# Kernel optimization log

Measured on AMD Instinct MI355X. Metric: run time of the kernel, lower is better.

Reference implementation:

```python
import jax, jax.numpy as jnp
import numpy as np

N_EMBDS = 1024
N_HEADS = 16
HEAD_DIM = N_EMBDS // N_HEADS


def setup_inputs() -> dict:
    key = jax.random.key(0)
    ks = jax.random.split(key, 5)
    B, T, C = 2, 2048, N_EMBDS
    x = jax.random.normal(ks[0], (B, T, C), dtype=jnp.float32)
    s = 1.0 / np.sqrt(C)
    W_attn = jax.random.normal(ks[1], (C, 3 * C), dtype=jnp.float32) * s
    b_attn = jnp.zeros((3 * C,), dtype=jnp.float32)
    W_proj = jax.random.normal(ks[2], (C, C), dtype=jnp.float32) * s
    b_proj = jnp.zeros((C,), dtype=jnp.float32)
    return {"x": x, "W_attn": W_attn, "b_attn": b_attn, "W_proj": W_proj, "b_proj": b_proj}


def reference(x, W_attn, b_attn, W_proj, b_proj):
    B, T, C = x.shape
    H, D = N_HEADS, HEAD_DIM
    qkv = x @ W_attn + b_attn  # [B, T, 3C]
    q, k, v = jnp.split(qkv, 3, axis=-1)
    # [B, H, T, D]
    q = q.reshape(B, T, H, D).transpose(0, 2, 1, 3)
    k = k.reshape(B, T, H, D).transpose(0, 2, 1, 3)
    v = v.reshape(B, T, H, D).transpose(0, 2, 1, 3)
    att = jnp.einsum('bhqd,bhkd->bhqk', q, k) * (1.0 / np.sqrt(D))  # [B,H,T,T]
    causal = jnp.tril(jnp.ones((T, T), dtype=bool))
    att = jnp.where(causal[None, None], att, -jnp.inf)
    att = jax.nn.softmax(att, axis=-1)
    y = jnp.einsum('bhqk,bhkd->bhqd', att, v)  # [B,H,T,D]
    y = y.transpose(0, 2, 1, 3).reshape(B, T, C)
    return y @ W_proj + b_proj
```

## Files before the change

### kernel.cpp

```cpp
#include <hip/hip_runtime.h>
#include <hip/hip_bf16.h>


typedef __bf16 bf16x8 __attribute__((ext_vector_type(8)));
typedef float  f32x4  __attribute__((ext_vector_type(4)));
#define BF16 __hip_bfloat16

constexpr int Bb = 2, Tt = 2048, Cc = 1024, Hh = 16, Dd = 64;
constexpr float NEG_INF = -1e30f;

__device__ __forceinline__ f32x4 mfma16(bf16x8 a, bf16x8 b, f32x4 c) {
  return __builtin_amdgcn_mfma_f32_16x16x32_bf16(a, b, c, 0, 0, 0);
}

__device__ __forceinline__ void gll16(const void* g, void* l) {
  __builtin_amdgcn_global_load_lds((const __attribute__((address_space(1))) void*)g,
                                   (__attribute__((address_space(3))) void*)l,
                                   16, 0, 0);
}

__device__ __forceinline__ int swz64(int r, int c) {
  return r * 64 + ((((c >> 3) ^ r) & 7) << 3) + (c & 7);
}

__device__ __forceinline__ int kperm(int kr) {
  return (((kr >> 5) << 1) + ((kr >> 2) & 1)) * 16 + (((kr >> 3) & 3) << 2) + (kr & 3);
}

__global__ void prep_kernel(const float* __restrict__ x, BF16* __restrict__ xb,
                            const float* __restrict__ Wa, BF16* __restrict__ WaT,
                            const float* __restrict__ Wp, BF16* __restrict__ WpT) {
  __shared__ float tile[32][33];
  const int bx = blockIdx.x, tid = threadIdx.x;
  if (bx < 2048) {
    const int i = (bx * 256 + tid) * 8;
    const float4 a = *(const float4*)&x[i];
    const float4 b = *(const float4*)&x[i + 4];
    BF16 o[8];
    o[0] = __float2bfloat16(a.x); o[1] = __float2bfloat16(a.y);
    o[2] = __float2bfloat16(a.z); o[3] = __float2bfloat16(a.w);
    o[4] = __float2bfloat16(b.x); o[5] = __float2bfloat16(b.y);
    o[6] = __float2bfloat16(b.z); o[7] = __float2bfloat16(b.w);
    *(uint4*)&xb[i] = *(const uint4*)o;
    return;
  }
  const float* in; BF16* outT; int K, N, gx, gy;
  if (bx < 5120) {
    const int idx = bx - 2048;
    in = Wa; outT = WaT; K = 1024; N = 3072; gx = idx % 96; gy = idx / 96;
  } else {
    const int idx = bx - 5120;
    in = Wp; outT = WpT; K = 1024; N = 1024; gx = idx % 32; gy = idx / 32;
  }
  const int n0 = gx * 32, k0 = gy * 32;
  const int tx = tid & 31, ty = tid >> 5;
#pragma unroll
  for (int i = ty; i < 32; i += 8) tile[i][tx] = in[(size_t)(k0 + i) * N + (n0 + tx)];
  __syncthreads();
#pragma unroll
  for (int i = ty; i < 32; i += 8)
    outT[(size_t)(n0 + i) * K + (k0 + tx)] = __float2bfloat16(tile[tx][i]);
}

__global__ void transpose_v(const BF16* __restrict__ in, BF16* __restrict__ out) {
  __shared__ BF16 tile[32][33];
  const int t0 = blockIdx.x * 32, d0 = blockIdx.y * 32, bh = blockIdx.z;
  const BF16* src = in + (size_t)bh * Tt * Dd;
  BF16* dst = out + (size_t)bh * Tt * Dd;
  const int tx = threadIdx.x, ty = threadIdx.y;
#pragma unroll
  for (int i = ty; i < 32; i += 8) tile[i][tx] = src[(size_t)(t0 + i) * Dd + (d0 + tx)];
  __syncthreads();
#pragma unroll
  for (int i = ty; i < 32; i += 8) dst[(size_t)(d0 + i) * Tt + (t0 + tx)] = tile[tx][i];
}

template <int MODE>
__global__ __launch_bounds__(256) void gemm_bt(const BF16* __restrict__ A,
                                               const BF16* __restrict__ Bt,
                                               const float* __restrict__ bias,
                                               BF16* __restrict__ oq,
                                               BF16* __restrict__ ok,
                                               BF16* __restrict__ ov,
                                               float* __restrict__ fout,
                                               int Ndim, int Kdim) {
  __shared__ alignas(16) BF16 sA[128 * 32];
  __shared__ alignas(16) BF16 sB[128 * 32];
  const int tid = threadIdx.x;
  const int wave = tid >> 6, lane = tid & 63;
  const int quad = lane >> 4, l16 = lane & 15;
  const int wm = (wave >> 1) * 64, wn = (wave & 1) * 64;
  const int bm = blockIdx.y * 128, bn = blockIdx.x * 128;

  f32x4 acc[4][4];
#pragma unroll
  for (int i = 0; i < 4; ++i)
#pragma unroll
    for (int j = 0; j < 4; ++j) acc[i][j] = f32x4{0.f, 0.f, 0.f, 0.f};

  const int rowA = wave * 32 + (lane >> 2);
  const int sub8 = (lane & 3) * 8;
  const BF16* gA0 = &A[(size_t)(bm + rowA) * Kdim + sub8];
  const BF16* gB0 = &Bt[(size_t)(bn + rowA) * Kdim + sub8];
  const size_t rstep16 = (size_t)16 * Kdim;
  BF16* lA0 = &sA[wave * 1024];
  BF16* lA1 = &sA[wave * 1024 + 512];
  BF16* lB0 = &sB[wave * 1024];
  BF16* lB1 = &sB[wave * 1024 + 512];

  for (int k0 = 0; k0 < Kdim; k0 += 32) {
    __syncthreads();
    gll16(gA0 + k0, lA0);
    gll16(gA0 + rstep16 + k0, lA1);
    gll16(gB0 + k0, lB0);
    gll16(gB0 + rstep16 + k0, lB1);
    __syncthreads();

    bf16x8 af[4], bf_[4];
#pragma unroll
    for (int i = 0; i < 4; ++i)
      af[i] = *(const bf16x8*)&sA[(wm + i * 16 + l16) * 32 + quad * 8];
#pragma unroll
    for (int j = 0; j < 4; ++j)
      bf_[j] = *(const bf16x8*)&sB[(wn + j * 16 + l16) * 32 + quad * 8];
#pragma unroll
    for (int i = 0; i < 4; ++i)
#pragma unroll
      for (int j = 0; j < 4; ++j) acc[i][j] = mfma16(af[i], bf_[j], acc[i][j]);
  }

#pragma unroll
  for (int j = 0; j < 4; ++j) {
    const int gn = bn + wn + j * 16 + l16;
    const float bsv = bias[gn];
#pragma unroll
    for (int i = 0; i < 4; ++i) {
#pragma unroll
      for (int r = 0; r < 4; ++r) {
        const int gm = bm + wm + i * 16 + quad * 4 + r;
        float val = acc[i][j][r] + bsv;
        if (MODE == 0) {
          const int which = gn >> 10, c = gn & 1023;
          const int hh = c >> 6, dd = c & 63;
          const int bb = gm >> 11, tk = gm & 2047;
          if (which == 0) val *= 0.125f;
          BF16* dst = (which == 0) ? oq : (which == 1) ? ok : ov;
          dst[(((size_t)(bb * Hh + hh)) * Tt + tk) * Dd + dd] = __float2bfloat16(val);
        } else {
          fout[(size_t)gm * Ndim + gn] = val;
        }
      }
    }
  }
}

__global__ __launch_bounds__(256) void attn_kernel(const BF16* __restrict__ qg,
                                                   const BF16* __restrict__ kg,
                                                   const BF16* __restrict__ vtg,
                                                   BF16* __restrict__ yb) {
  __shared__ alignas(16) BF16 sK[64 * 64];
  __shared__ alignas(16) BF16 sV[64 * 64];
  const int pr = blockIdx.x, h = blockIdx.y, b = blockIdx.z;
  const int qt[2] = {pr, 31 - pr};
  const int tid = threadIdx.x;
  const int wave = tid >> 6, lane = tid & 63;
  const int quad = lane >> 4, l16 = lane & 15;
  const size_t base = ((size_t)(b * Hh + h)) * Tt * Dd;

  bf16x8 qf[2][2];
#pragma unroll
  for (int s = 0; s < 2; ++s) {
    const size_t off = base + (size_t)(qt[s] * 64 + wave * 16 + l16) * Dd;
    qf[s][0] = *(const bf16x8*)&qg[off + quad * 8];
    qf[s][1] = *(const bf16x8*)&qg[off + 32 + quad * 8];
  }

  bf16x8 ones8;
#pragma unroll
  for (int j = 0; j < 8; ++j) ones8[j] = (__bf16)1.0f;

  f32x4 o[2][4], oL[2];
#pragma unroll
  for (int s = 0; s < 2; ++s) {
#pragma unroll
    for (int i = 0; i < 4; ++i) o[s][i] = f32x4{0.f, 0.f, 0.f, 0.f};
    oL[s] = f32x4{0.f, 0.f, 0.f, 0.f};
  }

  const int krow = tid >> 2, kcg = (tid & 3) * 16;
  const int kprow = kperm(krow);

  for (int jt = 0; jt <= qt[1]; ++jt) {
    const int kb = jt * 64;
    __syncthreads();
    {
      const uint4* pk = (const uint4*)&kg[base + (size_t)(kb + krow) * Dd + kcg];
      const uint4* pv = (const uint4*)&vtg[base + (size_t)krow * Tt + kb + kcg];
      uint4 k0 = pk[0], k1 = pk[1];
      uint4 v0 = pv[0], v1 = pv[1];
      *(uint4*)&sK[swz64(kprow, kcg)]     = k0;
      *(uint4*)&sK[swz64(kprow, kcg + 8)] = k1;
      *(uint4*)&sV[swz64(krow, kcg)]      = v0;
      *(uint4*)&sV[swz64(krow, kcg + 8)]  = v1;
    }
    __syncthreads();

    const bool actA = (jt <= qt[0]);

    f32x4 sS[2][4];
#pragma unroll
    for (int t = 0; t < 4; ++t) {
      const bf16x8 kf0 = *(const bf16x8*)&sK[swz64(t * 16 + l16, quad * 8)];
      const bf16x8 kf1 = *(const bf16x8*)&sK[swz64(t * 16 + l16, 32 + quad * 8)];
      sS[1][t] = mfma16(kf0, qf[1][0], f32x4{0.f, 0.f, 0.f, 0.f});
      sS[1][t] = mfma16(kf1, qf[1][1], sS[1][t]);
      if (actA) {
        sS[0][t] = mfma16(kf0, qf[0][0], f32x4{0.f, 0.f, 0.f, 0.f});
        sS[0][t] = mfma16(kf1, qf[0][1], sS[0][t]);
      }
    }

    bf16x8 pf[2][2];
#pragma unroll
    for (int s = 0; s < 2; ++s) {
      if (s == 0 && !actA) continue;
      if (jt == qt[s]) {
        const int q = qt[s] * 64 + wave * 16 + l16;
#pragma unroll
        for (int t = 0; t < 4; ++t) {
          const int kc0 = kb + (t >> 1) * 32 + quad * 8 + (t & 1) * 4;
#pragma unroll
          for (int r = 0; r < 4; ++r)
            if (kc0 + r > q) sS[s][t][r] = NEG_INF;
        }
      }
#pragma unroll
      for (int cc = 0; cc < 2; ++cc)
#pragma unroll
        for (int j = 0; j < 8; ++j)
          pf[s][cc][j] = (__bf16)__expf(sS[s][cc * 2 + (j >> 2)][j & 3] - 12.0f);
    }

#pragma unroll
    for (int cc = 0; cc < 2; ++cc) {
#pragma unroll
      for (int dt = 0; dt < 4; ++dt) {
        const bf16x8 vb =
            *(const bf16x8*)&sV[swz64(dt * 16 + l16, cc * 32 + quad * 8)];
        o[1][dt] = mfma16(pf[1][cc], vb, o[1][dt]);
        if (actA) o[0][dt] = mfma16(pf[0][cc], vb, o[0][dt]);
      }
      oL[1] = mfma16(pf[1][cc], ones8, oL[1]);
      if (actA) oL[0] = mfma16(pf[0][cc], ones8, oL[0]);
    }
  }

#pragma unroll
  for (int s = 0; s < 2; ++s) {
#pragma unroll
    for (int r = 0; r < 4; ++r) {
      const float inv = 1.0f / oL[s][r];
      const int trow = qt[s] * 64 + wave * 16 + quad * 4 + r;
#pragma unroll
      for (int dt = 0; dt < 4; ++dt)
        yb[((size_t)(b * Tt + trow)) * Cc + h * Dd + dt * 16 + l16] =
            __float2bfloat16(o[s][dt][r] * inv);
    }
  }
}

extern "C" void kernel_launch(void* const* d_in, const int* in_sizes, int n_in,
                              void* d_out, int out_size, void* d_ws, size_t ws_size,
                              hipStream_t stream) {
  (void)in_sizes; (void)n_in; (void)out_size; (void)ws_size;
  const float* x      = (const float*)d_in[0];
  const float* W_attn = (const float*)d_in[1];
  const float* b_attn = (const float*)d_in[2];
  const float* W_proj = (const float*)d_in[3];
  const float* b_proj = (const float*)d_in[4];
  float* out = (float*)d_out;

  constexpr size_t SZ_WA = (size_t)3072 * 1024;
  constexpr size_t SZ_WP = (size_t)1024 * 1024;
  constexpr size_t SZ_X  = (size_t)4096 * 1024;
  constexpr size_t SZ_T  = (size_t)Bb * Hh * Tt * Dd;

  BF16* ws   = (BF16*)d_ws;
  BF16* wtAb = ws;
  BF16* wtPb = wtAb + SZ_WA;
  BF16* xb   = wtPb + SZ_WP;
  BF16* q    = xb + SZ_X;
  BF16* k    = q + SZ_T;
  BF16* v    = k + SZ_T;
  BF16* vt   = v + SZ_T;
  BF16* yb   = vt + SZ_T;

  prep_kernel<<<dim3(6144), 256, 0, stream>>>(x, xb, W_attn, wtAb, W_proj, wtPb);
  gemm_bt<0><<<dim3(24, 32), 256, 0, stream>>>(xb, wtAb, b_attn, q, k, v, nullptr,
                                               3072, 1024);
  transpose_v<<<dim3(64, 2, 32), dim3(32, 8), 0, stream>>>(v, vt);
  attn_kernel<<<dim3(16, 16, 2), 256, 0, stream>>>(q, k, vt, yb);
  gemm_bt<1><<<dim3(8, 32), 256, 0, stream>>>(yb, wtPb, b_proj, nullptr, nullptr,
                                              nullptr, out, 1024, 1024);
}
```

Before: 200.1 us.

## Split attention into 32-row query strips per wave pair and prefetch K/V into registers

```diff
diff --git a/kernel.cpp b/kernel.cpp
--- a/kernel.cpp
+++ b/kernel.cpp
@@ -161,85 +161,87 @@
   __shared__ alignas(16) BF16 sK[64 * 64];
   __shared__ alignas(16) BF16 sV[64 * 64];
   const int pr = blockIdx.x, h = blockIdx.y, b = blockIdx.z;
-  const int qt[2] = {pr, 31 - pr};
   const int tid = threadIdx.x;
   const int wave = tid >> 6, lane = tid & 63;
   const int quad = lane >> 4, l16 = lane & 15;
+  const int qs = (wave >> 1) ? (63 - pr) : pr;
+  const int sub = wave & 1;
+  const int jt_diag = qs >> 1;
+  const int jt_max = (63 - pr) >> 1;
   const size_t base = ((size_t)(b * Hh + h)) * Tt * Dd;
-
-  bf16x8 qf[2][2];
-#pragma unroll
-  for (int s = 0; s < 2; ++s) {
-    const size_t off = base + (size_t)(qt[s] * 64 + wave * 16 + l16) * Dd;
-    qf[s][0] = *(const bf16x8*)&qg[off + quad * 8];
-    qf[s][1] = *(const bf16x8*)&qg[off + 32 + quad * 8];
+  const int qrow0 = qs * 32 + sub * 16;
+
+  bf16x8 qf0, qf1;
+  {
+    const size_t off = base + (size_t)(qrow0 + l16) * Dd;
+    qf0 = *(const bf16x8*)&qg[off + quad * 8];
+    qf1 = *(const bf16x8*)&qg[off + 32 + quad * 8];
   }
 
   bf16x8 ones8;
 #pragma unroll
   for (int j = 0; j < 8; ++j) ones8[j] = (__bf16)1.0f;
 
-  f32x4 o[2][4], oL[2];
-#pragma unroll
-  for (int s = 0; s < 2; ++s) {
-#pragma unroll
-    for (int i = 0; i < 4; ++i) o[s][i] = f32x4{0.f, 0.f, 0.f, 0.f};
-    oL[s] = f32x4{0.f, 0.f, 0.f, 0.f};
-  }
+  f32x4 o[4], oL;
+#pragma unroll
+  for (int i = 0; i < 4; ++i) o[i] = f32x4{0.f, 0.f, 0.f, 0.f};
+  oL = f32x4{0.f, 0.f, 0.f, 0.f};
 
   const int krow = tid >> 2, kcg = (tid & 3) * 16;
   const int kprow = kperm(krow);
 
-  for (int jt = 0; jt <= qt[1]; ++jt) {
+  uint4 rk0, rk1, rv0, rv1;
+  {
+    const uint4* pk = (const uint4*)&kg[base + (size_t)krow * Dd + kcg];
+    const uint4* pv = (const uint4*)&vtg[base + (size_t)krow * Tt + kcg];
+    rk0 = pk[0]; rk1 = pk[1];
+    rv0 = pv[0]; rv1 = pv[1];
+  }
+
+  for (int jt = 0; jt <= jt_max; ++jt) {
+    __syncthreads();
+    *(uint4*)&sK[swz64(kprow, kcg)]     = rk0;
+    *(uint4*)&sK[swz64(kprow, kcg + 8)] = rk1;
+    *(uint4*)&sV[swz64(krow, kcg)]      = rv0;
+    *(uint4*)&sV[swz64(krow, kcg + 8)]  = rv1;
+    if (jt < jt_max) {
+      const int kb2 = (jt + 1) * 64;
+      const uint4* nk = (const uint4*)&kg[base + (size_t)(kb2 + krow) * Dd + kcg];
+      const uint4* nv = (const uint4*)&vtg[base + (size_t)krow * Tt + kb2 + kcg];
+      rk0 = nk[0]; rk1 = nk[1];
+      rv0 = nv[0]; rv1 = nv[1];
+    }
+    __syncthreads();
+
+    if (jt > jt_diag) continue;
     const int kb = jt * 64;
-    __syncthreads();
-    {
-      const uint4* pk = (const uint4*)&kg[base + (size_t)(kb + krow) * Dd + kcg];
-      const uint4* pv = (const uint4*)&vtg[base + (size_t)krow * Tt + kb + kcg];
-      uint4 k0 = pk[0], k1 = pk[1];
-      uint4 v0 = pv[0], v1 = pv[1];
-      *(uint4*)&sK[swz64(kprow, kcg)]     = k0;
-      *(uint4*)&sK[swz64(kprow, kcg + 8)] = k1;
-      *(uint4*)&sV[swz64(krow, kcg)]      = v0;
-      *(uint4*)&sV[swz64(krow, kcg + 8)]  = v1;
-    }
-    __syncthreads();
-
-    const bool actA = (jt <= qt[0]);
-
-    f32x4 sS[2][4];
+
+    f32x4 sS[4];
 #pragma unroll
     for (int t = 0; t < 4; ++t) {
       const bf16x8 kf0 = *(const bf16x8*)&sK[swz64(t * 16 + l16, quad * 8)];
       const bf16x8 kf1 = *(const bf16x8*)&sK[swz64(t * 16 + l16, 32 + quad * 8)];
-      sS[1][t] = mfma16(kf0, qf[1][0], f32x4{0.f, 0.f, 0.f, 0.f});
-      sS[1][t] = mfma16(kf1, qf[1][1], sS[1][t]);
-      if (actA) {
-        sS[0][t] = mfma16(kf0, qf[0][0], f32x4{0.f, 0.f, 0.f, 0.f});
-        sS[0][t] = mfma16(kf1, qf[0][1], sS[0][t]);
+      sS[t] = mfma16(kf0, qf0, f32x4{0.f, 0.f, 0.f, 0.f});
+      sS[t] = mfma16(kf1, qf1, sS[t]);
+    }
+
+    if (jt == jt_diag) {
+      const int q = qrow0 + l16;
+#pragma unroll
+      for (int t = 0; t < 4; ++t) {
+        const int kc0 = kb + (t >> 1) * 32 + quad * 8 + (t & 1) * 4;
+#pragma unroll
+        for (int r = 0; r < 4; ++r)
+          if (kc0 + r > q) sS[t][r] = NEG_INF;
       }
     }
 
-    bf16x8 pf[2][2];
-#pragma unroll
-    for (int s = 0; s < 2; ++s) {
-      if (s == 0 && !actA) continue;
-      if (jt == qt[s]) {
-        const int q = qt[s] * 64 + wave * 16 + l16;
-#pragma unroll
-        for (int t = 0; t < 4; ++t) {
-          const int kc0 = kb + (t >> 1) * 32 + quad * 8 + (t & 1) * 4;
-#pragma unroll
-          for (int r = 0; r < 4; ++r)
-            if (kc0 + r > q) sS[s][t][r] = NEG_INF;
-        }
-      }
-#pragma unroll
-      for (int cc = 0; cc < 2; ++cc)
-#pragma unroll
-        for (int j = 0; j < 8; ++j)
-          pf[s][cc][j] = (__bf16)__expf(sS[s][cc * 2 + (j >> 2)][j & 3] - 12.0f);
-    }
+    bf16x8 pf[2];
+#pragma unroll
+    for (int cc = 0; cc < 2; ++cc)
+#pragma unroll
+      for (int j = 0; j < 8; ++j)
+        pf[cc][j] = (__bf16)__expf(sS[cc * 2 + (j >> 2)][j & 3] - 12.0f);
 
 #pragma unroll
     for (int cc = 0; cc < 2; ++cc) {
@@ -247,25 +249,20 @@
       for (int dt = 0; dt < 4; ++dt) {
         const bf16x8 vb =
             *(const bf16x8*)&sV[swz64(dt * 16 + l16, cc * 32 + quad * 8)];
-        o[1][dt] = mfma16(pf[1][cc], vb, o[1][dt]);
-        if (actA) o[0][dt] = mfma16(pf[0][cc], vb, o[0][dt]);
+        o[dt] = mfma16(pf[cc], vb, o[dt]);
       }
-      oL[1] = mfma16(pf[1][cc], ones8, oL[1]);
-      if (actA) oL[0] = mfma16(pf[0][cc], ones8, oL[0]);
-    }
-  }
-
-#pragma unroll
-  for (int s = 0; s < 2; ++s) {
-#pragma unroll
-    for (int r = 0; r < 4; ++r) {
-      const float inv = 1.0f / oL[s][r];
-      const int trow = qt[s] * 64 + wave * 16 + quad * 4 + r;
-#pragma unroll
-      for (int dt = 0; dt < 4; ++dt)
-        yb[((size_t)(b * Tt + trow)) * Cc + h * Dd + dt * 16 + l16] =
-            __float2bfloat16(o[s][dt][r] * inv);
-    }
+      oL = mfma16(pf[cc], ones8, oL);
+    }
+  }
+
+#pragma unroll
+  for (int r = 0; r < 4; ++r) {
+    const float inv = 1.0f / oL[r];
+    const int trow = qrow0 + quad * 4 + r;
+#pragma unroll
+    for (int dt = 0; dt < 4; ++dt)
+      yb[((size_t)(b * Tt + trow)) * Cc + h * Dd + dt * 16 + l16] =
+          __float2bfloat16(o[dt][r] * inv);
   }
 }
 
@@ -299,7 +296,7 @@
   gemm_bt<0><<<dim3(24, 32), 256, 0, stream>>>(xb, wtAb, b_attn, q, k, v, nullptr,
                                                3072, 1024);
   transpose_v<<<dim3(64, 2, 32), dim3(32, 8), 0, stream>>>(v, vt);
-  attn_kernel<<<dim3(16, 16, 2), 256, 0, stream>>>(q, k, vt, yb);
+  attn_kernel<<<dim3(32, 16, 2), 256, 0, stream>>>(q, k, vt, yb);
   gemm_bt<1><<<dim3(8, 32), 256, 0, stream>>>(yb, wtPb, b_proj, nullptr, nullptr,
                                               nullptr, out, 1024, 1024);
 }
```

Result: faster. 193.4 us (-3.4%).
